# Optimization experiments

Measured on AMD Instinct MI355X. Metric: run time of the kernel, lower is better.

The kernel has to match this reference:

```python
import jax, jax.numpy as jnp
import numpy as np

EPS = 1e-3
LOG2PI = float(np.log(2.0 * np.pi))

# dims
B, Z, Y, T, D = 32768, 256, 32, 64, 4  # batch, z_dim, y_dim, n_types, type_dim


def setup_inputs() -> dict:
    key = jax.random.key(0)
    ks = jax.random.split(key, 8)
    z = jax.random.normal(ks[0], (B, Z), dtype=jnp.float32)
    batch_x = jax.random.normal(ks[1], (B, T, D), dtype=jnp.float32)
    miss_list = jax.random.randint(ks[2], (B, T), 0, 2, dtype=jnp.int32)  # 1=observed, 0=missing
    data_mean = jax.random.normal(ks[3], (T, D), dtype=jnp.float32)
    data_var = jax.random.uniform(ks[4], (T, D), dtype=jnp.float32, minval=0.5, maxval=1.5)
    # weights init N(0, 0.005) as in the torch module; biases zero
    Wy = jax.random.normal(ks[5], (T * Y, Z), dtype=jnp.float32) * 0.005
    by = jnp.zeros((T * Y,), dtype=jnp.float32)
    Wm = jax.random.normal(ks[6], (T, D, Y), dtype=jnp.float32) * 0.005
    bm = jnp.zeros((T, D), dtype=jnp.float32)
    Wv = jax.random.normal(ks[7], (T, D, Y), dtype=jnp.float32) * 0.005
    bv = jnp.zeros((T, D), dtype=jnp.float32)
    return {"z": z, "batch_x": batch_x, "miss_list": miss_list,
            "data_mean": data_mean, "data_var": data_var,
            "Wy": Wy, "by": by, "Wm": Wm, "bm": bm, "Wv": Wv, "bv": bv}


def reference(z, batch_x, miss_list, data_mean, data_var, Wy, by, Wm, bm, Wv, bv):
    # y_layer: z -> [B, T*Y], grouped into per-type gamma slices [B, T, Y]
    y = z @ Wy.T + by
    gamma = y.reshape(y.shape[0], T, Y)

    mask = miss_list.astype(gamma.dtype)            # [B, T], 1=observed
    m3 = mask[:, :, None]                           # [B, T, 1]

    # per-type tiny linears (dynamic_partition + Linear + dynamic_stitch).
    # Numerically: same linear on all rows; missing rows are under no_grad,
    # realized here as stop_gradient on the missing partition.
    lin_m = jnp.einsum('bty,tdy->btd', gamma, Wm) + bm   # [B, T, D]
    lin_v = jnp.einsum('bty,tdy->btd', gamma, Wv) + bv
    est_mean = m3 * lin_m + (1.0 - m3) * jax.lax.stop_gradient(lin_m)
    est_var_raw = m3 * lin_v + (1.0 - m3) * jax.lax.stop_gradient(lin_v)

    # loglik_real: softplus variance, denormalize with data mean/var
    dvar = jnp.clip(data_var, EPS)
    est_var = jnp.clip(jax.nn.softplus(est_var_raw), EPS, 1e20)
    mean_x = jnp.sqrt(dvar) * est_mean + data_mean       # [B, T, D]
    var_x = dvar * est_var                               # [B, T, D]

    log_p = -0.5 * jnp.sum((batch_x - mean_x) ** 2 / var_x + jnp.log(var_x) + LOG2PI, axis=-1)  # [B, T]
    log_p_x = log_p * mask
    log_p_x_missing = log_p * (1.0 - mask)
    return (log_p_x, log_p_x_missing, mean_x, var_x)
```

## Files before the change

kernel.cpp:

```cpp
#include <hip/hip_runtime.h>


#define Bsz   32768
#define Tsz   64
#define Dsz   4
#define Ysz   32
#define Zsz   256
#define Nsz   512
#define BTtot (Bsz * Tsz)
#define EPS_  1e-3f
#define LOG2PI_ 1.8378770664093453f

#define BM       64
#define NT       512
#define ASTRIDE  264
#define LSTRIDE  528

typedef __attribute__((ext_vector_type(4))) float  f32x4;
typedef __attribute__((ext_vector_type(8))) short  short8;
typedef __attribute__((ext_vector_type(2))) unsigned int uint2v;

static __device__ __forceinline__ unsigned short f2bf(float f) {
    unsigned int u = __float_as_uint(f);
    return (unsigned short)((u + 0x7fffu + ((u >> 16) & 1u)) >> 16);
}
static __device__ __forceinline__ float bf2f(unsigned short h) {
    return __uint_as_float(((unsigned int)h) << 16);
}

__global__ __launch_bounds__(256)
void hidec_prep(const float* __restrict__ Wy, const float* __restrict__ by,
                const float* __restrict__ Wm, const float* __restrict__ bm,
                const float* __restrict__ Wv, const float* __restrict__ bv,
                unsigned short* __restrict__ weff, float* __restrict__ beff) {
    __shared__ float Ml[8][Ysz];
    __shared__ float byl[Ysz];
    const int t   = blockIdx.x;
    const int tid = threadIdx.x;
    {
        int j = tid >> 5, y = tid & 31;
        const float* src = (j < 4) ? Wm : Wv;
        Ml[j][y] = src[(t * Dsz + (j & 3)) * Ysz + y];
    }
    if (tid < Ysz) byl[tid] = by[t * Ysz + tid];
    __syncthreads();

    const int k = tid;
    const int kk = k >> 5, q = (k >> 3) & 3, je = k & 7;
    float wy[Ysz];
#pragma unroll
    for (int y = 0; y < Ysz; ++y)
        wy[y] = Wy[(size_t)(t * Ysz + y) * Zsz + k];
#pragma unroll
    for (int j = 0; j < 8; ++j) {
        float acc = 0.f;
#pragma unroll
        for (int y = 0; y < Ysz; ++y) acc = fmaf(Ml[j][y], wy[y], acc);
        int n   = t * 8 + j;
        int tau = n >> 4, c = n & 15;
        weff[((((tau * 8 + kk) * 4 + q) * 16 + c) * 8) + je] = f2bf(acc);
    }
    if (tid < 8) {
        int d = tid & 3;
        float s = ((tid < 4) ? bm : bv)[t * Dsz + d];
        for (int y = 0; y < Ysz; ++y) s = fmaf(byl[y], Ml[tid][y], s);
        beff[t * 8 + tid] = s;
    }
}

__global__ __launch_bounds__(NT, 4)
void hidec_main(const float* __restrict__ z, const float* __restrict__ bx,
                const int* __restrict__ miss, const float* __restrict__ dmean,
                const float* __restrict__ dvarp, const unsigned short* __restrict__ weff,
                const float* __restrict__ beff, float* __restrict__ out) {
    __shared__ unsigned short buf[BM * ASTRIDE];
    __shared__ float4 sqA[Tsz], dmA[Tsz], dcA[Tsz];
    __shared__ float  sldv[Tsz];
    __shared__ float  beffL[Nsz];

    const int tid  = threadIdx.x;
    const long row0 = (long)blockIdx.x * BM;

    if (tid < Tsz) {
        float4 dv4 = *(const float4*)(dvarp + tid * 4);
        float4 dm4 = *(const float4*)(dmean + tid * 4);
        float d0 = fmaxf(dv4.x, EPS_), d1 = fmaxf(dv4.y, EPS_);
        float d2 = fmaxf(dv4.z, EPS_), d3 = fmaxf(dv4.w, EPS_);
        sqA[tid] = (float4){sqrtf(d0), sqrtf(d1), sqrtf(d2), sqrtf(d3)};
        dmA[tid] = dm4;
        dcA[tid] = (float4){d0, d1, d2, d3};
        sldv[tid] = __logf(d0) + __logf(d1) + __logf(d2) + __logf(d3);
    }
    beffL[tid] = beff[tid];

    unsigned short* a_lds = buf;
#pragma unroll
    for (int i = 0; i < 8; ++i) {
        int idx4 = tid + i * NT;
        int r  = idx4 >> 6;
        int c4 = idx4 & 63;
        float4 v = *(const float4*)(z + (row0 + r) * Zsz + c4 * 4);
        uint2v p;
        p.x = (unsigned)f2bf(v.x) | ((unsigned)f2bf(v.y) << 16);
        p.y = (unsigned)f2bf(v.z) | ((unsigned)f2bf(v.w) << 16);
        *(uint2v*)&a_lds[r * ASTRIDE + c4 * 4] = p;
    }
    __syncthreads();

    const int lane = tid & 63;
    const int w    = tid >> 6;
    const int c    = lane & 15;
    const int q    = lane >> 4;

    f32x4 acc[16];
#pragma unroll
    for (int i = 0; i < 16; ++i) acc[i] = (f32x4){0.f, 0.f, 0.f, 0.f};

    const unsigned short* wp = weff + ((size_t)(w * 4) * 8) * 512 + lane * 8;

#pragma unroll
    for (int kk = 0; kk < 8; ++kk) {
        short8 b0 = *(const short8*)(wp + kk * 512 + 0 * 4096);
        short8 b1 = *(const short8*)(wp + kk * 512 + 1 * 4096);
        short8 b2 = *(const short8*)(wp + kk * 512 + 2 * 4096);
        short8 b3 = *(const short8*)(wp + kk * 512 + 3 * 4096);
        short8 a0 = *(const short8*)&a_lds[(0 * 16 + c) * ASTRIDE + kk * 32 + q * 8];
        short8 a1 = *(const short8*)&a_lds[(1 * 16 + c) * ASTRIDE + kk * 32 + q * 8];
        short8 a2 = *(const short8*)&a_lds[(2 * 16 + c) * ASTRIDE + kk * 32 + q * 8];
        short8 a3 = *(const short8*)&a_lds[(3 * 16 + c) * ASTRIDE + kk * 32 + q * 8];
        acc[0]  = __builtin_amdgcn_mfma_f32_16x16x32_bf16(a0, b0, acc[0],  0, 0, 0);
        acc[1]  = __builtin_amdgcn_mfma_f32_16x16x32_bf16(a1, b0, acc[1],  0, 0, 0);
        acc[2]  = __builtin_amdgcn_mfma_f32_16x16x32_bf16(a2, b0, acc[2],  0, 0, 0);
        acc[3]  = __builtin_amdgcn_mfma_f32_16x16x32_bf16(a3, b0, acc[3],  0, 0, 0);
        acc[4]  = __builtin_amdgcn_mfma_f32_16x16x32_bf16(a0, b1, acc[4],  0, 0, 0);
        acc[5]  = __builtin_amdgcn_mfma_f32_16x16x32_bf16(a1, b1, acc[5],  0, 0, 0);
        acc[6]  = __builtin_amdgcn_mfma_f32_16x16x32_bf16(a2, b1, acc[6],  0, 0, 0);
        acc[7]  = __builtin_amdgcn_mfma_f32_16x16x32_bf16(a3, b1, acc[7],  0, 0, 0);
        acc[8]  = __builtin_amdgcn_mfma_f32_16x16x32_bf16(a0, b2, acc[8],  0, 0, 0);
        acc[9]  = __builtin_amdgcn_mfma_f32_16x16x32_bf16(a1, b2, acc[9],  0, 0, 0);
        acc[10] = __builtin_amdgcn_mfma_f32_16x16x32_bf16(a2, b2, acc[10], 0, 0, 0);
        acc[11] = __builtin_amdgcn_mfma_f32_16x16x32_bf16(a3, b2, acc[11], 0, 0, 0);
        acc[12] = __builtin_amdgcn_mfma_f32_16x16x32_bf16(a0, b3, acc[12], 0, 0, 0);
        acc[13] = __builtin_amdgcn_mfma_f32_16x16x32_bf16(a1, b3, acc[13], 0, 0, 0);
        acc[14] = __builtin_amdgcn_mfma_f32_16x16x32_bf16(a2, b3, acc[14], 0, 0, 0);
        acc[15] = __builtin_amdgcn_mfma_f32_16x16x32_bf16(a3, b3, acc[15], 0, 0, 0);
    }
    __syncthreads();

    unsigned short* lin = buf;
#pragma unroll
    for (int ch = 0; ch < 2; ++ch) {
#pragma unroll
        for (int ti = 0; ti < 4; ++ti) {
            int n  = (w * 4 + ti) * 16 + c;
            float bb = beffL[n];
            int t  = n >> 3;
            int jj = n & 7;
#pragma unroll
            for (int rh = 0; rh < 2; ++rh) {
                int rt = ch * 2 + rh;
#pragma unroll
                for (int reg = 0; reg < 4; ++reg) {
                    int rl = rh * 16 + q * 4 + reg;
                    lin[rl * LSTRIDE + t * 8 + jj] = f2bf(acc[ti * 4 + rt][reg] + bb);
                }
            }
        }
        __syncthreads();

#pragma unroll
        for (int pp = 0; pp < 4; ++pp) {
            int task = pp * NT + tid;
            int t  = task & 63;
            int rl = task >> 6;
            long bt = (row0 + ch * 32 + rl) * Tsz + t;

            short8 l8 = *(const short8*)&lin[rl * LSTRIDE + t * 8];
            float lm[4], lv[4];
#pragma unroll
            for (int d = 0; d < 4; ++d) {
                lm[d] = bf2f((unsigned short)l8[d]);
                lv[d] = bf2f((unsigned short)l8[4 + d]);
            }

            float4 x4  = *(const float4*)(bx + bt * 4);
            float4 sq4 = sqA[t];
            float4 dm4 = dmA[t];
            float4 dc4 = dcA[t];
            float xa[4]  = {x4.x,  x4.y,  x4.z,  x4.w};
            float sqa[4] = {sq4.x, sq4.y, sq4.z, sq4.w};
            float dma[4] = {dm4.x, dm4.y, dm4.z, dm4.w};
            float dca[4] = {dc4.x, dc4.y, dc4.z, dc4.w};

            float mean_o[4], var_o[4];
            float s = sldv[t];
            float evp = 1.f;
#pragma unroll
            for (int d = 0; d < 4; ++d) {
                float mean = fmaf(sqa[d], lm[d], dma[d]);
                float v    = lv[d];
                float sp   = fmaxf(v, 0.f) + __logf(1.f + __expf(-fabsf(v)));
                float ev   = fminf(fmaxf(sp, EPS_), 1e20f);
                float var  = dca[d] * ev;
                float diff = xa[d] - mean;
                s = fmaf(diff * diff, __builtin_amdgcn_rcpf(var), s);
                evp *= ev;
                mean_o[d] = mean;
                var_o[d]  = var;
            }
            s += __logf(evp);
            float logp = -0.5f * (s + 4.f * LOG2PI_);
            float mk = (float)miss[bt];

            float lx = logp * mk;
            out[bt]         = lx;
            out[BTtot + bt] = logp - lx;

            *(float4*)(out + 2L * BTtot + bt * 4) =
                (float4){mean_o[0], mean_o[1], mean_o[2], mean_o[3]};
            *(float4*)(out + 6L * BTtot + bt * 4) =
                (float4){var_o[0], var_o[1], var_o[2], var_o[3]};
        }
        __syncthreads();
    }
}

extern "C" void kernel_launch(void* const* d_in, const int* in_sizes, int n_in,
                              void* d_out, int out_size, void* d_ws, size_t ws_size,
                              hipStream_t stream) {
    const float* z     = (const float*)d_in[0];
    const float* bx    = (const float*)d_in[1];
    const int*   miss  = (const int*)d_in[2];
    const float* dmean = (const float*)d_in[3];
    const float* dvar  = (const float*)d_in[4];
    const float* Wy    = (const float*)d_in[5];
    const float* by    = (const float*)d_in[6];
    const float* Wm    = (const float*)d_in[7];
    const float* bm    = (const float*)d_in[8];
    const float* Wv    = (const float*)d_in[9];
    const float* bv    = (const float*)d_in[10];
    float* out = (float*)d_out;

    unsigned short* weff = (unsigned short*)d_ws;
    float* beff = (float*)((char*)d_ws + (size_t)Nsz * Zsz * 2);

    hidec_prep<<<Tsz, Zsz, 0, stream>>>(Wy, by, Wm, bm, Wv, bv, weff, beff);
    hidec_main<<<Bsz / BM, NT, 0, stream>>>(z, bx, miss, dmean, dvar, weff, beff, out);
}
```

Baseline: 175.3 us.

## Shrink row tile to 32 rows with 4 waves each covering 128 columns

Result: slower. 184.3 us (+5.2%).

```diff
diff --git a/kernel.cpp b/kernel.cpp
--- a/kernel.cpp
+++ b/kernel.cpp
@@ -11,10 +11,10 @@
 #define EPS_  1e-3f
 #define LOG2PI_ 1.8378770664093453f
 
-#define BM       64
-#define NT       512
+#define BM       32
+#define NT       256
 #define ASTRIDE  264
-#define LSTRIDE  528
+#define LSTRIDE  520
 
 typedef __attribute__((ext_vector_type(4))) float  f32x4;
 typedef __attribute__((ext_vector_type(8))) short  short8;
@@ -73,7 +73,7 @@
                 const int* __restrict__ miss, const float* __restrict__ dmean,
                 const float* __restrict__ dvarp, const unsigned short* __restrict__ weff,
                 const float* __restrict__ beff, float* __restrict__ out) {
-    __shared__ unsigned short buf[BM * ASTRIDE];
+    __shared__ unsigned short buf[BM * LSTRIDE];
     __shared__ float4 sqA[Tsz], dmA[Tsz], dcA[Tsz];
     __shared__ float  sldv[Tsz];
     __shared__ float  beffL[Nsz];
@@ -91,7 +91,8 @@
         dcA[tid] = (float4){d0, d1, d2, d3};
         sldv[tid] = __logf(d0) + __logf(d1) + __logf(d2) + __logf(d3);
     }
-    beffL[tid] = beff[tid];
+    beffL[tid]       = beff[tid];
+    beffL[tid + 256] = beff[tid + 256];
 
     unsigned short* a_lds = buf;
 #pragma unroll
@@ -116,112 +117,91 @@
 #pragma unroll
     for (int i = 0; i < 16; ++i) acc[i] = (f32x4){0.f, 0.f, 0.f, 0.f};
 
-    const unsigned short* wp = weff + ((size_t)(w * 4) * 8) * 512 + lane * 8;
+    const unsigned short* wp = weff + (size_t)w * 32768 + lane * 8;
 
 #pragma unroll
     for (int kk = 0; kk < 8; ++kk) {
-        short8 b0 = *(const short8*)(wp + kk * 512 + 0 * 4096);
-        short8 b1 = *(const short8*)(wp + kk * 512 + 1 * 4096);
-        short8 b2 = *(const short8*)(wp + kk * 512 + 2 * 4096);
-        short8 b3 = *(const short8*)(wp + kk * 512 + 3 * 4096);
         short8 a0 = *(const short8*)&a_lds[(0 * 16 + c) * ASTRIDE + kk * 32 + q * 8];
         short8 a1 = *(const short8*)&a_lds[(1 * 16 + c) * ASTRIDE + kk * 32 + q * 8];
-        short8 a2 = *(const short8*)&a_lds[(2 * 16 + c) * ASTRIDE + kk * 32 + q * 8];
-        short8 a3 = *(const short8*)&a_lds[(3 * 16 + c) * ASTRIDE + kk * 32 + q * 8];
-        acc[0]  = __builtin_amdgcn_mfma_f32_16x16x32_bf16(a0, b0, acc[0],  0, 0, 0);
-        acc[1]  = __builtin_amdgcn_mfma_f32_16x16x32_bf16(a1, b0, acc[1],  0, 0, 0);
-        acc[2]  = __builtin_amdgcn_mfma_f32_16x16x32_bf16(a2, b0, acc[2],  0, 0, 0);
-        acc[3]  = __builtin_amdgcn_mfma_f32_16x16x32_bf16(a3, b0, acc[3],  0, 0, 0);
-        acc[4]  = __builtin_amdgcn_mfma_f32_16x16x32_bf16(a0, b1, acc[4],  0, 0, 0);
-        acc[5]  = __builtin_amdgcn_mfma_f32_16x16x32_bf16(a1, b1, acc[5],  0, 0, 0);
-        acc[6]  = __builtin_amdgcn_mfma_f32_16x16x32_bf16(a2, b1, acc[6],  0, 0, 0);
-        acc[7]  = __builtin_amdgcn_mfma_f32_16x16x32_bf16(a3, b1, acc[7],  0, 0, 0);
-        acc[8]  = __builtin_amdgcn_mfma_f32_16x16x32_bf16(a0, b2, acc[8],  0, 0, 0);
-        acc[9]  = __builtin_amdgcn_mfma_f32_16x16x32_bf16(a1, b2, acc[9],  0, 0, 0);
-        acc[10] = __builtin_amdgcn_mfma_f32_16x16x32_bf16(a2, b2, acc[10], 0, 0, 0);
-        acc[11] = __builtin_amdgcn_mfma_f32_16x16x32_bf16(a3, b2, acc[11], 0, 0, 0);
-        acc[12] = __builtin_amdgcn_mfma_f32_16x16x32_bf16(a0, b3, acc[12], 0, 0, 0);
-        acc[13] = __builtin_amdgcn_mfma_f32_16x16x32_bf16(a1, b3, acc[13], 0, 0, 0);
-        acc[14] = __builtin_amdgcn_mfma_f32_16x16x32_bf16(a2, b3, acc[14], 0, 0, 0);
-        acc[15] = __builtin_amdgcn_mfma_f32_16x16x32_bf16(a3, b3, acc[15], 0, 0, 0);
+#pragma unroll
+        for (int ti = 0; ti < 8; ++ti) {
+            short8 b = *(const short8*)(wp + (size_t)(ti * 8 + kk) * 512);
+            acc[ti * 2 + 0] = __builtin_amdgcn_mfma_f32_16x16x32_bf16(a0, b, acc[ti * 2 + 0], 0, 0, 0);
+            acc[ti * 2 + 1] = __builtin_amdgcn_mfma_f32_16x16x32_bf16(a1, b, acc[ti * 2 + 1], 0, 0, 0);
+        }
     }
     __syncthreads();
 
     unsigned short* lin = buf;
 #pragma unroll
-    for (int ch = 0; ch < 2; ++ch) {
-#pragma unroll
-        for (int ti = 0; ti < 4; ++ti) {
-            int n  = (w * 4 + ti) * 16 + c;
-            float bb = beffL[n];
-            int t  = n >> 3;
-            int jj = n & 7;
-#pragma unroll
-            for (int rh = 0; rh < 2; ++rh) {
-                int rt = ch * 2 + rh;
-#pragma unroll
-                for (int reg = 0; reg < 4; ++reg) {
-                    int rl = rh * 16 + q * 4 + reg;
-                    lin[rl * LSTRIDE + t * 8 + jj] = f2bf(acc[ti * 4 + rt][reg] + bb);
-                }
+    for (int ti = 0; ti < 8; ++ti) {
+        int n  = (w * 8 + ti) * 16 + c;
+        float bb = beffL[n];
+        int t  = n >> 3;
+        int jj = n & 7;
+#pragma unroll
+        for (int rt = 0; rt < 2; ++rt) {
+#pragma unroll
+            for (int reg = 0; reg < 4; ++reg) {
+                int rl = rt * 16 + q * 4 + reg;
+                lin[rl * LSTRIDE + t * 8 + jj] = f2bf(acc[ti * 2 + rt][reg] + bb);
             }
         }
-        __syncthreads();
-
-#pragma unroll
-        for (int pp = 0; pp < 4; ++pp) {
-            int task = pp * NT + tid;
-            int t  = task & 63;
-            int rl = task >> 6;
-            long bt = (row0 + ch * 32 + rl) * Tsz + t;
-
-            short8 l8 = *(const short8*)&lin[rl * LSTRIDE + t * 8];
-            float lm[4], lv[4];
-#pragma unroll
-            for (int d = 0; d < 4; ++d) {
-                lm[d] = bf2f((unsigned short)l8[d]);
-                lv[d] = bf2f((unsigned short)l8[4 + d]);
-            }
-
-            float4 x4  = *(const float4*)(bx + bt * 4);
-            float4 sq4 = sqA[t];
-            float4 dm4 = dmA[t];
-            float4 dc4 = dcA[t];
-            float xa[4]  = {x4.x,  x4.y,  x4.z,  x4.w};
-            float sqa[4] = {sq4.x, sq4.y, sq4.z, sq4.w};
-            float dma[4] = {dm4.x, dm4.y, dm4.z, dm4.w};
-            float dca[4] = {dc4.x, dc4.y, dc4.z, dc4.w};
-
-            float mean_o[4], var_o[4];
-            float s = sldv[t];
-            float evp = 1.f;
-#pragma unroll
-            for (int d = 0; d < 4; ++d) {
-                float mean = fmaf(sqa[d], lm[d], dma[d]);
-                float v    = lv[d];
-                float sp   = fmaxf(v, 0.f) + __logf(1.f + __expf(-fabsf(v)));
-                float ev   = fminf(fmaxf(sp, EPS_), 1e20f);
-                float var  = dca[d] * ev;
-                float diff = xa[d] - mean;
-                s = fmaf(diff * diff, __builtin_amdgcn_rcpf(var), s);
-                evp *= ev;
-                mean_o[d] = mean;
-                var_o[d]  = var;
-            }
-            s += __logf(evp);
-            float logp = -0.5f * (s + 4.f * LOG2PI_);
-            float mk = (float)miss[bt];
-
-            float lx = logp * mk;
-            out[bt]         = lx;
-            out[BTtot + bt] = logp - lx;
-
-            *(float4*)(out + 2L * BTtot + bt * 4) =
-                (float4){mean_o[0], mean_o[1], mean_o[2], mean_o[3]};
-            *(float4*)(out + 6L * BTtot + bt * 4) =
-                (float4){var_o[0], var_o[1], var_o[2], var_o[3]};
-        }
-        __syncthreads();
+    }
+    __syncthreads();
+
+#pragma unroll
+    for (int pp = 0; pp < 8; ++pp) {
+        int task = pp * NT + tid;
+        int t  = task & 63;
+        int rl = task >> 6;
+        long bt = (row0 + rl) * Tsz + t;
+
+        short8 l8 = *(const short8*)&lin[rl * LSTRIDE + t * 8];
+        float lm[4], lv[4];
+#pragma unroll
+        for (int d = 0; d < 4; ++d) {
+            lm[d] = bf2f((unsigned short)l8[d]);
+            lv[d] = bf2f((unsigned short)l8[4 + d]);
+        }
+
+        float4 x4  = *(const float4*)(bx + bt * 4);
+        float4 sq4 = sqA[t];
+        float4 dm4 = dmA[t];
+        float4 dc4 = dcA[t];
+        float xa[4]  = {x4.x,  x4.y,  x4.z,  x4.w};
+        float sqa[4] = {sq4.x, sq4.y, sq4.z, sq4.w};
+        float dma[4] = {dm4.x, dm4.y, dm4.z, dm4.w};
+        float dca[4] = {dc4.x, dc4.y, dc4.z, dc4.w};
+
+        float mean_o[4], var_o[4];
+        float s = sldv[t];
+        float evp = 1.f;
+#pragma unroll
+        for (int d = 0; d < 4; ++d) {
+            float mean = fmaf(sqa[d], lm[d], dma[d]);
+            float v    = lv[d];
+            float sp   = fmaxf(v, 0.f) + __logf(1.f + __expf(-fabsf(v)));
+            float ev   = fminf(fmaxf(sp, EPS_), 1e20f);
+            float var  = dca[d] * ev;
+            float diff = xa[d] - mean;
+            s = fmaf(diff * diff, __builtin_amdgcn_rcpf(var), s);
+            evp *= ev;
+            mean_o[d] = mean;
+            var_o[d]  = var;
+        }
+        s += __logf(evp);
+        float logp = -0.5f * (s + 4.f * LOG2PI_);
+        float mk = (float)miss[bt];
+
+        float lx = logp * mk;
+        out[bt]         = lx;
+        out[BTtot + bt] = logp - lx;
+
+        *(float4*)(out + 2L * BTtot + bt * 4) =
+            (float4){mean_o[0], mean_o[1], mean_o[2], mean_o[3]};
+        *(float4*)(out + 6L * BTtot + bt * 4) =
+            (float4){var_o[0], var_o[1], var_o[2], var_o[3]};
     }
 }
 
```
